# Kernel tuning notes

Hardware: AMD Instinct MI355X
Metric: run time of the kernel (lower is better)

Reference implementation:

```python
import jax, jax.numpy as jnp
import numpy as np

LEAK = 0.2
N, C, T, H, DOUT = 512, 16, 15, 32, 32


def setup_inputs() -> dict:
    key = jax.random.key(0)
    k = jax.random.split(key, 5)
    x = jax.random.normal(k[0], (N, C), dtype=jnp.float32)
    adj = jax.random.uniform(k[1], (N, N, T), dtype=jnp.float32)
    W1 = jax.random.normal(k[2], (2 * C, T + 1, H), dtype=jnp.float32) * 0.05
    W2 = jax.random.normal(k[3], (2 * C, T + 1, DOUT), dtype=jnp.float32) * 0.05
    W3 = jax.random.normal(k[4], (C, H), dtype=jnp.float32) * 0.05
    return {"x": x, "adj": adj, "W1": W1, "W2": W2, "W3": W3}


def reference(x, adj, W1, W2, W3):
    n, c = x.shape
    # input_diag: [N,N,C,1], diagonal copy of node features
    diag = jnp.einsum('mn,ni->mni', jnp.eye(n, dtype=x.dtype), x)[..., None]
    # D = concat(adj-weighted broadcast of x, diag) along edge-type axis -> [N,N,C,T+1]
    D = jnp.concatenate([jnp.einsum('mnt,ni->mnit', adj, x), diag], axis=3)
    # symmetrize along channel axis -> [N,N,2C,T+1]
    D = jnp.concatenate([D, jnp.transpose(D, (1, 0, 2, 3))], axis=2)
    K = jnp.einsum('mnit,ith->mnh', D, W1)   # [N,N,H]
    V = jnp.einsum('mnit,itd->mnd', D, W2)   # [N,N,DOUT]
    Q = x @ W3                               # [N,H]
    logits1 = jnp.einsum('nh,nmh->nm', Q, K)
    logits2 = jnp.einsum('mh,nmh->nm', Q, K)
    s1 = jax.nn.softmax(logits1, axis=1)
    s2 = jax.nn.softmax(logits2, axis=0)
    temp = jnp.einsum('nm,nmd->nd', s1, V) + jnp.einsum('nm,nmd->md', s2, V)
    return jnp.maximum(temp, LEAK * temp)  # lrelu
```

## Files before the change

kernel.cpp:

```cpp
#include <hip/hip_runtime.h>
#include <hip/hip_bf16.h>

#define NNODE 512
#define CCH   16
#define TT    15
#define TP    16
#define HH    32
#define DD    32

typedef unsigned short u16;
typedef unsigned int   u32;
typedef short bf8 __attribute__((ext_vector_type(8)));
typedef float f4  __attribute__((ext_vector_type(4)));

__device__ __forceinline__ float bf2f(u16 v) {
    union { u32 u; float f; } x; x.u = ((u32)v) << 16; return x.f;
}
__device__ __forceinline__ u16 f2bf(float f) {
    union { float f; u32 u; } x; x.f = f;
    u32 u = x.u;
    return (u16)((u + 0x7FFFu + ((u >> 16) & 1u)) >> 16);
}
__device__ __forceinline__ void unpack8(uint4 p, float* o) {
    o[0]=bf2f((u16)(p.x & 0xffffu)); o[1]=bf2f((u16)(p.x >> 16));
    o[2]=bf2f((u16)(p.y & 0xffffu)); o[3]=bf2f((u16)(p.y >> 16));
    o[4]=bf2f((u16)(p.z & 0xffffu)); o[5]=bf2f((u16)(p.z >> 16));
    o[6]=bf2f((u16)(p.w & 0xffffu)); o[7]=bf2f((u16)(p.w >> 16));
}
__device__ __forceinline__ uint4 pack8(const u16* v) {
    return make_uint4((u32)v[0]|((u32)v[1]<<16), (u32)v[2]|((u32)v[3]<<16),
                      (u32)v[4]|((u32)v[5]<<16), (u32)v[6]|((u32)v[7]<<16));
}

__global__ __launch_bounds__(256) void k_prep_adjp(
    const float* __restrict__ x, const float* __restrict__ W1,
    const float* __restrict__ W2, const float* __restrict__ W3,
    const float* __restrict__ adj,
    u16* __restrict__ A1, u16* __restrict__ B1,
    u16* __restrict__ A2, u16* __restrict__ B2,
    u16* __restrict__ A2T, u16* __restrict__ B2T,
    u16* __restrict__ Qb, float* __restrict__ QAd, float* __restrict__ QB,
    u16* __restrict__ adjP, u16* __restrict__ adjPT)
{
    int tid = threadIdx.x;
    if (blockIdx.x < 512) {
        int n = blockIdx.x;
        __shared__ alignas(16) float xs[CCH];
        __shared__ alignas(16) float A1row[512], B1row[512];
        __shared__ alignas(16) float A2row[512], B2row[512];
        __shared__ alignas(16) float Qs[HH];
        if (tid < CCH) xs[tid] = x[n*CCH + tid];
        __syncthreads();
        float xr[CCH];
        #pragma unroll
        for (int i=0;i<CCH;i++) xr[i]=xs[i];
        #pragma unroll
        for (int rep=0; rep<2; rep++) {
            int c = tid + rep*256;
            float a1=0.f,b1=0.f,a2=0.f,b2=0.f;
            #pragma unroll
            for (int i=0;i<CCH;i++) {
                a1 += xr[i]*W1[i*512 + c];
                b1 += xr[i]*W1[(CCH+i)*512 + c];
                a2 += xr[i]*W2[i*512 + c];
                b2 += xr[i]*W2[(CCH+i)*512 + c];
            }
            A1[(size_t)n*512 + c]=f2bf(a1); B1[(size_t)n*512 + c]=f2bf(b1);
            A2[(size_t)n*512 + c]=f2bf(a2); B2[(size_t)n*512 + c]=f2bf(b2);
            A1row[c]=a1; B1row[c]=b1; A2row[c]=a2; B2row[c]=b2;
        }
        if (tid < HH) {
            float q=0.f;
            #pragma unroll
            for (int i=0;i<CCH;i++) q += xr[i]*W3[i*HH + tid];
            Qs[tid]=q; Qb[(size_t)n*HH + tid]=f2bf(q);
        }
        __syncthreads();
        if (tid < TP) {
            float qa=0.f, qb=0.f;
            #pragma unroll
            for (int h=0;h<HH;h++) { qa += Qs[h]*A1row[tid*HH+h]; qb += Qs[h]*B1row[tid*HH+h]; }
            QAd[(size_t)n*TP + tid]=qa; QB[(size_t)n*TP + tid]=qb;
        }
        {
            int d = tid >> 3, t0 = (tid & 7) * 2;
            u32 pa = (u32)f2bf(A2row[t0*32 + d]) | ((u32)f2bf(A2row[(t0+1)*32 + d]) << 16);
            u32 pb = (u32)f2bf(B2row[t0*32 + d]) | ((u32)f2bf(B2row[(t0+1)*32 + d]) << 16);
            *(u32*)(A2T + (size_t)d*8192 + n*16 + t0) = pa;
            *(u32*)(B2T + (size_t)d*8192 + n*16 + t0) = pb;
        }
    } else {
        int b = blockIdx.x - 512;
        int n0 = (b >> 4) * 32, m0 = (b & 15) * 32;
        __shared__ alignas(16) u16 s[32*520];
        #pragma unroll
        for (int i = 0; i < 60; i++) {
            int e = tid + i*256;
            int nl = e / 480; int rem = e - nl*480;
            int ml = rem / 15; int t = rem - ml*15;
            float v = adj[((size_t)(n0+nl)*512 + (m0+ml))*TT + t];
            s[nl*520 + ml*16 + t] = f2bf(v);
        }
        #pragma unroll
        for (int i = 0; i < 4; i++) {
            int e = tid + i*256; int nl = e >> 5, ml = e & 31;
            s[nl*520 + ml*16 + 15] = ((n0+nl) == (m0+ml)) ? (u16)0x3F80 : (u16)0;
        }
        __syncthreads();
        #pragma unroll
        for (int i = 0; i < 8; i++) {
            int c = tid + i*256;
            int nl = c >> 6, off = (c & 63) * 8;
            uint4 vv = *(const uint4*)(s + nl*520 + off);
            *(uint4*)(adjP + (size_t)(n0+nl)*8192 + m0*16 + off) = vv;
        }
        #pragma unroll
        for (int i = 0; i < 8; i++) {
            int c = tid + i*256;
            int ml = c >> 6, nlh = c & 63, nl = nlh >> 1, half = nlh & 1;
            uint4 vv = *(const uint4*)(s + nl*520 + ml*16 + half*8);
            *(uint4*)(adjPT + (size_t)(m0+ml)*8192 + (n0+nl)*16 + half*8) = vv;
        }
    }
}

__global__ __launch_bounds__(256) void k_logits(
    const u16* __restrict__ Qb, const u16* __restrict__ A1, const u16* __restrict__ B1,
    const u16* __restrict__ adjP, const u16* __restrict__ adjPT,
    const float* __restrict__ QAd, const float* __restrict__ QB,
    float* __restrict__ L1, float* __restrict__ L2T)
{
    const int m0 = blockIdx.x * 16, n0 = blockIdx.y * 16;
    const int tid = threadIdx.x;
    const int wv = tid >> 6, lane = tid & 63, l15 = lane & 15, quad = lane >> 4;
    __shared__ alignas(16) float sL1[16*17];
    __shared__ alignas(16) float sL2[16*17];

    bf8 afragN = *(const bf8*)(Qb + (size_t)(n0 + l15)*32 + quad*8);
    bf8 afragM = *(const bf8*)(Qb + (size_t)(m0 + l15)*32 + quad*8);

    f4 accG[4], accH[4];
    #pragma unroll
    for (int j = 0; j < 4; j++) {
        int m = m0 + wv*4 + j;
        int n = n0 + wv*4 + j;
        bf8 bG = *(const bf8*)(A1 + (size_t)m*512 + l15*32 + quad*8);
        bf8 bH = *(const bf8*)(B1 + (size_t)n*512 + l15*32 + quad*8);
        f4 z = {0.f,0.f,0.f,0.f};
        accG[j] = __builtin_amdgcn_mfma_f32_16x16x32_bf16(afragN, bG, z, 0, 0, 0);
        accH[j] = __builtin_amdgcn_mfma_f32_16x16x32_bf16(afragM, bH, z, 0, 0, 0);
    }

    #pragma unroll
    for (int j = 0; j < 4; j++) {
        int m = m0 + wv*4 + j;
        #pragma unroll
        for (int r = 0; r < 4; r++) {
            int n = n0 + quad*4 + r;
            float a  = bf2f(adjP [(size_t)n*8192 + m*16 + l15]);
            float at = bf2f(adjPT[(size_t)n*8192 + m*16 + l15]);
            float v = a*accG[j][r] + at*QB[n*16 + l15];
            #pragma unroll
            for (int o = 1; o < 16; o <<= 1) v += __shfl_xor(v, o, 64);
            if (l15 == 0) sL1[(quad*4+r)*17 + wv*4 + j] = v;
        }
    }
    #pragma unroll
    for (int j = 0; j < 4; j++) {
        int n = n0 + wv*4 + j;
        #pragma unroll
        for (int r = 0; r < 4; r++) {
            int m = m0 + quad*4 + r;
            float a  = bf2f(adjP [(size_t)n*8192 + m*16 + l15]);
            float at = bf2f(adjPT[(size_t)n*8192 + m*16 + l15]);
            float v = a*QAd[m*16 + l15] + at*accH[j][r];
            #pragma unroll
            for (int o = 1; o < 16; o <<= 1) v += __shfl_xor(v, o, 64);
            if (l15 == 0) sL2[(quad*4+r)*17 + wv*4 + j] = v;
        }
    }
    __syncthreads();
    int row = tid >> 4, col = tid & 15;
    L1 [(size_t)(n0+row)*NNODE + m0 + col] = sL1[row*17+col];
    L2T[(size_t)(m0+row)*NNODE + n0 + col] = sL2[row*17+col];
}

__global__ __launch_bounds__(256) void k_softmax_w(
    const float* __restrict__ L1, const float* __restrict__ L2T,
    const u16* __restrict__ adjP, const u16* __restrict__ adjPT,
    u16* __restrict__ W1c, u16* __restrict__ W2c,
    float* __restrict__ u1, float* __restrict__ v2)
{
    int b = blockIdx.x, tid = threadIdx.x;
    bool first = b < NNODE;
    int j = first ? b : b - NNODE;
    const float* row = first ? (L1 + (size_t)j*NNODE) : (L2T + (size_t)j*NNODE);
    u16* W  = (first ? W1c : W2c) + (size_t)j*8192;
    float* uv = (first ? u1 : v2) + (size_t)j*TP;

    float v0 = row[tid], v1 = row[tid+256];
    float mx = fmaxf(v0, v1);
    #pragma unroll
    for (int o=32; o; o>>=1) mx = fmaxf(mx, __shfl_xor(mx, o, 64));
    __shared__ alignas(16) float red[4], red2[4], ur[4][16];
    int lane = tid & 63, wv = tid >> 6;
    if (!lane) red[wv] = mx;
    __syncthreads();
    mx = fmaxf(fmaxf(red[0],red[1]), fmaxf(red[2],red[3]));
    float e0 = __expf(v0 - mx), e1 = __expf(v1 - mx);
    float sm = e0 + e1;
    #pragma unroll
    for (int o=32; o; o>>=1) sm += __shfl_xor(sm, o, 64);
    if (!lane) red2[wv] = sm;
    __syncthreads();
    float inv = 1.0f / (red2[0]+red2[1]+red2[2]+red2[3]);
    float sa = e0*inv, sb = e1*inv;

    const u16* ap = adjP  + (size_t)j*8192;
    const u16* tp = adjPT + (size_t)j*8192;
    float u[16];
    #pragma unroll
    for (int t=0;t<16;t++) u[t]=0.f;
    #pragma unroll
    for (int half = 0; half < 2; half++) {
        int k = tid + half*256;
        float sv = half ? sb : sa;
        const uint4* p = (const uint4*)(ap + k*16);
        float av[16]; unpack8(p[0], av); unpack8(p[1], av+8);
        u16 o16[16];
        #pragma unroll
        for (int t=0;t<16;t++) o16[t] = f2bf(sv*av[t]);
        uint4* wp = (uint4*)(W + k*16);
        wp[0] = pack8(o16); wp[1] = pack8(o16+8);
        const uint4* q = (const uint4*)(tp + k*16);
        float tv[16]; unpack8(q[0], tv); unpack8(q[1], tv+8);
        #pragma unroll
        for (int t=0;t<16;t++) u[t] = fmaf(sv, tv[t], u[t]);
    }
    #pragma unroll
    for (int t=0;t<16;t++) {
        #pragma unroll
        for (int o=32; o; o>>=1) u[t] += __shfl_xor(u[t], o, 64);
    }
    if (!lane) {
        #pragma unroll
        for (int t=0;t<16;t++) ur[wv][t] = u[t];
    }
    __syncthreads();
    if (tid < 16) uv[tid] = ur[0][tid]+ur[1][tid]+ur[2][tid]+ur[3][tid];
}

__global__ __launch_bounds__(256) void k_gemm2(
    const u16* __restrict__ W1c, const u16* __restrict__ W2c,
    const u16* __restrict__ A2T, const u16* __restrict__ B2T,
    float* __restrict__ tempP)
{
    int tid = threadIdx.x;
    int wv = tid >> 6, lane = tid & 63, l15 = lane & 15, quad = lane >> 4;
    int w = blockIdx.x*4 + wv;
    int kc = w & 15, dt = (w >> 4) & 1, jt = w >> 5;
    size_t aRow = (size_t)(jt*16 + l15)*8192;
    size_t bRow = (size_t)(dt*16 + l15)*8192;
    int kt0 = kc*512 + quad*8;
    f4 acc = {0.f, 0.f, 0.f, 0.f};
    #pragma unroll
    for (int s = 0; s < 16; s++) {
        int kt = kt0 + s*32;
        bf8 aw1 = *(const bf8*)(W1c + aRow + kt);
        bf8 ba2 = *(const bf8*)(A2T + bRow + kt);
        acc = __builtin_amdgcn_mfma_f32_16x16x32_bf16(aw1, ba2, acc, 0, 0, 0);
        bf8 aw2 = *(const bf8*)(W2c + aRow + kt);
        bf8 bb2 = *(const bf8*)(B2T + bRow + kt);
        acc = __builtin_amdgcn_mfma_f32_16x16x32_bf16(aw2, bb2, acc, 0, 0, 0);
    }
    #pragma unroll
    for (int r = 0; r < 4; r++)
        tempP[((size_t)kc*NNODE + jt*16 + quad*4 + r)*DD + dt*16 + l15] = acc[r];
}

__global__ __launch_bounds__(256) void k_final(
    const float* __restrict__ tempP, const float* __restrict__ u1, const float* __restrict__ v2,
    const u16* __restrict__ A2, const u16* __restrict__ B2, float* __restrict__ out)
{
    int j0 = blockIdx.x * 8;
    int tid = threadIdx.x;
    int j = tid >> 5, d = tid & 31;
    int jj = j0 + j;
    float acc = 0.f;
    #pragma unroll
    for (int kc=0;kc<16;kc++) acc += tempP[((size_t)kc*NNODE + jj)*DD + d];
    #pragma unroll
    for (int t=0;t<TP;t++) {
        acc += u1[(size_t)jj*TP + t] * bf2f(B2[(size_t)jj*512 + t*32 + d]);
        acc += v2[(size_t)jj*TP + t] * bf2f(A2[(size_t)jj*512 + t*32 + d]);
    }
    out[(size_t)jj*DD + d] = fmaxf(acc, 0.2f*acc);
}

extern "C" void kernel_launch(void* const* d_in, const int* in_sizes, int n_in,
                              void* d_out, int out_size, void* d_ws, size_t ws_size,
                              hipStream_t stream)
{
    (void)in_sizes; (void)n_in; (void)out_size; (void)ws_size;
    const float* x   = (const float*)d_in[0];
    const float* adj = (const float*)d_in[1];
    const float* W1  = (const float*)d_in[2];
    const float* W2  = (const float*)d_in[3];
    const float* W3  = (const float*)d_in[4];

    char* ws = (char*)d_ws;
    u16*   adjP = (u16*)(ws);
    u16*   adjPT= (u16*)(ws + 0x800000);
    u16*   W1c  = (u16*)(ws + 0x1000000);
    u16*   W2c  = (u16*)(ws + 0x1800000);
    u16*   A1   = (u16*)(ws + 0x2000000);
    u16*   B1   = (u16*)(ws + 0x2080000);
    u16*   A2   = (u16*)(ws + 0x2100000);
    u16*   B2   = (u16*)(ws + 0x2180000);
    u16*   A2T  = (u16*)(ws + 0x2200000);
    u16*   B2T  = (u16*)(ws + 0x2280000);
    u16*   Qb   = (u16*)(ws + 0x2300000);
    float* QAd  = (float*)(ws + 0x2310000);
    float* QB   = (float*)(ws + 0x2320000);
    float* u1   = (float*)(ws + 0x2330000);
    float* v2   = (float*)(ws + 0x2340000);
    float* L1   = (float*)(ws + 0x2400000);
    float* L2T  = (float*)(ws + 0x2500000);
    float* tempP= (float*)(ws + 0x2600000);

    k_prep_adjp<<<768, 256, 0, stream>>>(x, W1, W2, W3, adj,
                                         A1, B1, A2, B2, A2T, B2T, Qb, QAd, QB, adjP, adjPT);
    k_logits<<<dim3(32,32), 256, 0, stream>>>(Qb, A1, B1, adjP, adjPT, QAd, QB, L1, L2T);
    k_softmax_w<<<1024, 256, 0, stream>>>(L1, L2T, adjP, adjPT, W1c, W2c, u1, v2);
    k_gemm2<<<256, 256, 0, stream>>>(W1c, W2c, A2T, B2T, tempP);
    k_final<<<64, 256, 0, stream>>>(tempP, u1, v2, A2, B2, (float*)d_out);
}
```

Before: 115.5 us.

## Fuse all stages into one cooperative kernel with grid-wide syncs

Merges the prep, logits, softmax-weighting, GEMM and final epilogue kernels into a single persistent cooperative kernel with 512 blocks, separated by grid.sync. The goal is to remove kernel launch gaps and the tempP partial-sum buffer, computing the self term from the A2T/B2T layout instead of separate A2/B2 arrays. In exchange, the final GEMM runs on only 16 blocks, each with a long serial K loop and no split-K. This may leave the machine underused and limit bandwidth while streaming the large W1c/W2c matrices.

```diff
diff --git a/kernel.cpp b/kernel.cpp
--- a/kernel.cpp
+++ b/kernel.cpp
@@ -1,5 +1,8 @@
 #include <hip/hip_runtime.h>
 #include <hip/hip_bf16.h>
+#include <hip/hip_cooperative_groups.h>
+
+namespace cg = cooperative_groups;
 
 #define NNODE 512
 #define CCH   16
@@ -32,23 +35,33 @@
                       (u32)v[4]|((u32)v[5]<<16), (u32)v[6]|((u32)v[7]<<16));
 }
 
-__global__ __launch_bounds__(256) void k_prep_adjp(
-    const float* __restrict__ x, const float* __restrict__ W1,
-    const float* __restrict__ W2, const float* __restrict__ W3,
-    const float* __restrict__ adj,
+__global__ __launch_bounds__(256, 2) void k_fused(
+    const float* __restrict__ x, const float* __restrict__ adj,
+    const float* __restrict__ W1, const float* __restrict__ W2,
+    const float* __restrict__ W3,
     u16* __restrict__ A1, u16* __restrict__ B1,
-    u16* __restrict__ A2, u16* __restrict__ B2,
     u16* __restrict__ A2T, u16* __restrict__ B2T,
     u16* __restrict__ Qb, float* __restrict__ QAd, float* __restrict__ QB,
-    u16* __restrict__ adjP, u16* __restrict__ adjPT)
+    u16* __restrict__ adjP, u16* __restrict__ adjPT,
+    float* __restrict__ L1, float* __restrict__ L2T,
+    u16* __restrict__ W1c, u16* __restrict__ W2c,
+    float* __restrict__ u1, float* __restrict__ v2,
+    float* __restrict__ out)
 {
-    int tid = threadIdx.x;
-    if (blockIdx.x < 512) {
-        int n = blockIdx.x;
-        __shared__ alignas(16) float xs[CCH];
-        __shared__ alignas(16) float A1row[512], B1row[512];
-        __shared__ alignas(16) float A2row[512], B2row[512];
-        __shared__ alignas(16) float Qs[HH];
+    cg::grid_group grid = cg::this_grid();
+    const int tid = threadIdx.x;
+    const int b = blockIdx.x;
+    __shared__ alignas(16) u16 sbuf[32*520];
+    float* fb = (float*)sbuf;
+
+    {
+        int n = b;
+        float* xs    = fb;
+        float* Qs    = fb + 16;
+        float* A1row = fb + 48;
+        float* B1row = fb + 560;
+        float* A2row = fb + 1072;
+        float* B2row = fb + 1584;
         if (tid < CCH) xs[tid] = x[n*CCH + tid];
         __syncthreads();
         float xr[CCH];
@@ -66,7 +79,6 @@
                 b2 += xr[i]*W2[(CCH+i)*512 + c];
             }
             A1[(size_t)n*512 + c]=f2bf(a1); B1[(size_t)n*512 + c]=f2bf(b1);
-            A2[(size_t)n*512 + c]=f2bf(a2); B2[(size_t)n*512 + c]=f2bf(b2);
             A1row[c]=a1; B1row[c]=b1; A2row[c]=a2; B2row[c]=b2;
         }
         if (tid < HH) {
@@ -89,212 +101,202 @@
             *(u32*)(A2T + (size_t)d*8192 + n*16 + t0) = pa;
             *(u32*)(B2T + (size_t)d*8192 + n*16 + t0) = pb;
         }
-    } else {
-        int b = blockIdx.x - 512;
-        int n0 = (b >> 4) * 32, m0 = (b & 15) * 32;
-        __shared__ alignas(16) u16 s[32*520];
-        #pragma unroll
-        for (int i = 0; i < 60; i++) {
-            int e = tid + i*256;
-            int nl = e / 480; int rem = e - nl*480;
-            int ml = rem / 15; int t = rem - ml*15;
-            float v = adj[((size_t)(n0+nl)*512 + (m0+ml))*TT + t];
-            s[nl*520 + ml*16 + t] = f2bf(v);
-        }
-        #pragma unroll
-        for (int i = 0; i < 4; i++) {
-            int e = tid + i*256; int nl = e >> 5, ml = e & 31;
-            s[nl*520 + ml*16 + 15] = ((n0+nl) == (m0+ml)) ? (u16)0x3F80 : (u16)0;
-        }
         __syncthreads();
-        #pragma unroll
-        for (int i = 0; i < 8; i++) {
-            int c = tid + i*256;
-            int nl = c >> 6, off = (c & 63) * 8;
-            uint4 vv = *(const uint4*)(s + nl*520 + off);
-            *(uint4*)(adjP + (size_t)(n0+nl)*8192 + m0*16 + off) = vv;
-        }
-        #pragma unroll
-        for (int i = 0; i < 8; i++) {
-            int c = tid + i*256;
-            int ml = c >> 6, nlh = c & 63, nl = nlh >> 1, half = nlh & 1;
-            uint4 vv = *(const uint4*)(s + nl*520 + ml*16 + half*8);
-            *(uint4*)(adjPT + (size_t)(m0+ml)*8192 + (n0+nl)*16 + half*8) = vv;
+        if (b < 256) {
+            int n0 = (b >> 4) * 32, m0 = (b & 15) * 32;
+            u16* s = sbuf;
+            #pragma unroll
+            for (int i = 0; i < 60; i++) {
+                int e = tid + i*256;
+                int nl = e / 480; int rem = e - nl*480;
+                int ml = rem / 15; int t = rem - ml*15;
+                float v = adj[((size_t)(n0+nl)*512 + (m0+ml))*TT + t];
+                s[nl*520 + ml*16 + t] = f2bf(v);
+            }
+            #pragma unroll
+            for (int i = 0; i < 4; i++) {
+                int e = tid + i*256; int nl = e >> 5, ml = e & 31;
+                s[nl*520 + ml*16 + 15] = ((n0+nl) == (m0+ml)) ? (u16)0x3F80 : (u16)0;
+            }
+            __syncthreads();
+            #pragma unroll
+            for (int i = 0; i < 8; i++) {
+                int c = tid + i*256;
+                int nl = c >> 6, off = (c & 63) * 8;
+                uint4 vv = *(const uint4*)(s + nl*520 + off);
+                *(uint4*)(adjP + (size_t)(n0+nl)*8192 + m0*16 + off) = vv;
+            }
+            #pragma unroll
+            for (int i = 0; i < 8; i++) {
+                int c = tid + i*256;
+                int ml = c >> 6, nlh = c & 63, nl = nlh >> 1, half = nlh & 1;
+                uint4 vv = *(const uint4*)(s + nl*520 + ml*16 + half*8);
+                *(uint4*)(adjPT + (size_t)(m0+ml)*8192 + (n0+nl)*16 + half*8) = vv;
+            }
         }
     }
-}
-
-__global__ __launch_bounds__(256) void k_logits(
-    const u16* __restrict__ Qb, const u16* __restrict__ A1, const u16* __restrict__ B1,
-    const u16* __restrict__ adjP, const u16* __restrict__ adjPT,
-    const float* __restrict__ QAd, const float* __restrict__ QB,
-    float* __restrict__ L1, float* __restrict__ L2T)
-{
-    const int m0 = blockIdx.x * 16, n0 = blockIdx.y * 16;
-    const int tid = threadIdx.x;
-    const int wv = tid >> 6, lane = tid & 63, l15 = lane & 15, quad = lane >> 4;
-    __shared__ alignas(16) float sL1[16*17];
-    __shared__ alignas(16) float sL2[16*17];
-
-    bf8 afragN = *(const bf8*)(Qb + (size_t)(n0 + l15)*32 + quad*8);
-    bf8 afragM = *(const bf8*)(Qb + (size_t)(m0 + l15)*32 + quad*8);
-
-    f4 accG[4], accH[4];
-    #pragma unroll
-    for (int j = 0; j < 4; j++) {
-        int m = m0 + wv*4 + j;
-        int n = n0 + wv*4 + j;
-        bf8 bG = *(const bf8*)(A1 + (size_t)m*512 + l15*32 + quad*8);
-        bf8 bH = *(const bf8*)(B1 + (size_t)n*512 + l15*32 + quad*8);
-        f4 z = {0.f,0.f,0.f,0.f};
-        accG[j] = __builtin_amdgcn_mfma_f32_16x16x32_bf16(afragN, bG, z, 0, 0, 0);
-        accH[j] = __builtin_amdgcn_mfma_f32_16x16x32_bf16(afragM, bH, z, 0, 0, 0);
+    grid.sync();
+
+    {
+        const int wv = tid >> 6, lane = tid & 63, l15 = lane & 15, quad = lane >> 4;
+        float* sL1 = fb;
+        float* sL2 = fb + 16*17;
+        #pragma unroll
+        for (int it = 0; it < 2; it++) {
+            __syncthreads();
+            int tile = b + it*512;
+            int m0 = (tile & 31) * 16, n0 = (tile >> 5) * 16;
+
+            bf8 afragN = *(const bf8*)(Qb + (size_t)(n0 + l15)*32 + quad*8);
+            bf8 afragM = *(const bf8*)(Qb + (size_t)(m0 + l15)*32 + quad*8);
+            f4 accG[4], accH[4];
+            #pragma unroll
+            for (int j = 0; j < 4; j++) {
+                int m = m0 + wv*4 + j;
+                int n = n0 + wv*4 + j;
+                bf8 bG = *(const bf8*)(A1 + (size_t)m*512 + l15*32 + quad*8);
+                bf8 bH = *(const bf8*)(B1 + (size_t)n*512 + l15*32 + quad*8);
+                f4 z = {0.f,0.f,0.f,0.f};
+                accG[j] = __builtin_amdgcn_mfma_f32_16x16x32_bf16(afragN, bG, z, 0, 0, 0);
+                accH[j] = __builtin_amdgcn_mfma_f32_16x16x32_bf16(afragM, bH, z, 0, 0, 0);
+            }
+            #pragma unroll
+            for (int j = 0; j < 4; j++) {
+                int m = m0 + wv*4 + j;
+                #pragma unroll
+                for (int r = 0; r < 4; r++) {
+                    int n = n0 + quad*4 + r;
+                    float a  = bf2f(adjP [(size_t)n*8192 + m*16 + l15]);
+                    float at = bf2f(adjPT[(size_t)n*8192 + m*16 + l15]);
+                    float v = a*accG[j][r] + at*QB[n*16 + l15];
+                    #pragma unroll
+                    for (int o = 1; o < 16; o <<= 1) v += __shfl_xor(v, o, 64);
+                    if (l15 == 0) sL1[(quad*4+r)*17 + wv*4 + j] = v;
+                }
+            }
+            #pragma unroll
+            for (int j = 0; j < 4; j++) {
+                int n = n0 + wv*4 + j;
+                #pragma unroll
+                for (int r = 0; r < 4; r++) {
+                    int m = m0 + quad*4 + r;
+                    float a  = bf2f(adjP [(size_t)n*8192 + m*16 + l15]);
+                    float at = bf2f(adjPT[(size_t)n*8192 + m*16 + l15]);
+                    float v = a*QAd[m*16 + l15] + at*accH[j][r];
+                    #pragma unroll
+                    for (int o = 1; o < 16; o <<= 1) v += __shfl_xor(v, o, 64);
+                    if (l15 == 0) sL2[(quad*4+r)*17 + wv*4 + j] = v;
+                }
+            }
+            __syncthreads();
+            int row = tid >> 4, col = tid & 15;
+            L1 [(size_t)(n0+row)*NNODE + m0 + col] = sL1[row*17+col];
+            L2T[(size_t)(m0+row)*NNODE + n0 + col] = sL2[row*17+col];
+        }
     }
-
-    #pragma unroll
-    for (int j = 0; j < 4; j++) {
-        int m = m0 + wv*4 + j;
+    grid.sync();
+
+    {
+        int lane = tid & 63, wv = tid >> 6;
+        float* red  = fb;
+        float* red2 = fb + 4;
+        float (*ur)[16] = (float(*)[16])(fb + 8);
+        #pragma unroll
+        for (int rr = 0; rr < 2; rr++) {
+            __syncthreads();
+            int task = b + rr*512;
+            bool first = task < NNODE;
+            int j = first ? task : task - NNODE;
+            const float* row = first ? (L1 + (size_t)j*NNODE) : (L2T + (size_t)j*NNODE);
+            u16* W  = (first ? W1c : W2c) + (size_t)j*8192;
+            float* uv = (first ? u1 : v2) + (size_t)j*TP;
+
+            float v0 = row[tid], v1 = row[tid+256];
+            float mx = fmaxf(v0, v1);
+            #pragma unroll
+            for (int o=32; o; o>>=1) mx = fmaxf(mx, __shfl_xor(mx, o, 64));
+            if (!lane) red[wv] = mx;
+            __syncthreads();
+            mx = fmaxf(fmaxf(red[0],red[1]), fmaxf(red[2],red[3]));
+            float e0 = __expf(v0 - mx), e1 = __expf(v1 - mx);
+            float sm = e0 + e1;
+            #pragma unroll
+            for (int o=32; o; o>>=1) sm += __shfl_xor(sm, o, 64);
+            if (!lane) red2[wv] = sm;
+            __syncthreads();
+            float inv = 1.0f / (red2[0]+red2[1]+red2[2]+red2[3]);
+            float sa = e0*inv, sb = e1*inv;
+
+            const u16* ap = adjP  + (size_t)j*8192;
+            const u16* tp = adjPT + (size_t)j*8192;
+            float u[16];
+            #pragma unroll
+            for (int t=0;t<16;t++) u[t]=0.f;
+            #pragma unroll
+            for (int half = 0; half < 2; half++) {
+                int k = tid + half*256;
+                float sv = half ? sb : sa;
+                const uint4* p = (const uint4*)(ap + k*16);
+                float av[16]; unpack8(p[0], av); unpack8(p[1], av+8);
+                u16 o16[16];
+                #pragma unroll
+                for (int t=0;t<16;t++) o16[t] = f2bf(sv*av[t]);
+                uint4* wp = (uint4*)(W + k*16);
+                wp[0] = pack8(o16); wp[1] = pack8(o16+8);
+                const uint4* q = (const uint4*)(tp + k*16);
+                float tv[16]; unpack8(q[0], tv); unpack8(q[1], tv+8);
+                #pragma unroll
+                for (int t=0;t<16;t++) u[t] = fmaf(sv, tv[t], u[t]);
+            }
+            #pragma unroll
+            for (int t=0;t<16;t++) {
+                #pragma unroll
+                for (int o=32; o; o>>=1) u[t] += __shfl_xor(u[t], o, 64);
+            }
+            if (!lane) {
+                #pragma unroll
+                for (int t=0;t<16;t++) ur[wv][t] = u[t];
+            }
+            __syncthreads();
+            if (tid < 16) uv[tid] = ur[0][tid]+ur[1][tid]+ur[2][tid]+ur[3][tid];
+        }
+    }
+    grid.sync();
+
+    if (b < 16) {
+        int wv = tid >> 6, lane = tid & 63, l15 = lane & 15, quad = lane >> 4;
+        int w = b*4 + wv;
+        int jt = w >> 1, dt = w & 1;
+        size_t aRow = (size_t)(jt*16 + l15)*8192;
+        size_t bRow = (size_t)(dt*16 + l15)*8192;
+        f4 acc = {0.f, 0.f, 0.f, 0.f};
+        #pragma unroll 8
+        for (int s = 0; s < 256; s++) {
+            int kt = s*32 + quad*8;
+            bf8 aw1 = *(const bf8*)(W1c + aRow + kt);
+            bf8 ba2 = *(const bf8*)(A2T + bRow + kt);
+            acc = __builtin_amdgcn_mfma_f32_16x16x32_bf16(aw1, ba2, acc, 0, 0, 0);
+            bf8 aw2 = *(const bf8*)(W2c + aRow + kt);
+            bf8 bb2 = *(const bf8*)(B2T + bRow + kt);
+            acc = __builtin_amdgcn_mfma_f32_16x16x32_bf16(aw2, bb2, acc, 0, 0, 0);
+        }
+        int d = dt*16 + l15;
         #pragma unroll
         for (int r = 0; r < 4; r++) {
-            int n = n0 + quad*4 + r;
-            float a  = bf2f(adjP [(size_t)n*8192 + m*16 + l15]);
-            float at = bf2f(adjPT[(size_t)n*8192 + m*16 + l15]);
-            float v = a*accG[j][r] + at*QB[n*16 + l15];
-            #pragma unroll
-            for (int o = 1; o < 16; o <<= 1) v += __shfl_xor(v, o, 64);
-            if (l15 == 0) sL1[(quad*4+r)*17 + wv*4 + j] = v;
+            int j = jt*16 + quad*4 + r;
+            const uint4* pb2 = (const uint4*)(B2T + (size_t)d*8192 + j*16);
+            const uint4* pa2 = (const uint4*)(A2T + (size_t)d*8192 + j*16);
+            float bv[16], av[16];
+            unpack8(pb2[0], bv); unpack8(pb2[1], bv+8);
+            unpack8(pa2[0], av); unpack8(pa2[1], av+8);
+            float self = 0.f;
+            #pragma unroll
+            for (int t = 0; t < 16; t++)
+                self += u1[(size_t)j*TP + t]*bv[t] + v2[(size_t)j*TP + t]*av[t];
+            float val = acc[r] + self;
+            out[(size_t)j*DD + d] = fmaxf(val, 0.2f*val);
         }
     }
-    #pragma unroll
-    for (int j = 0; j < 4; j++) {
-        int n = n0 + wv*4 + j;
-        #pragma unroll
-        for (int r = 0; r < 4; r++) {
-            int m = m0 + quad*4 + r;
-            float a  = bf2f(adjP [(size_t)n*8192 + m*16 + l15]);
-            float at = bf2f(adjPT[(size_t)n*8192 + m*16 + l15]);
-            float v = a*QAd[m*16 + l15] + at*accH[j][r];
-            #pragma unroll
-            for (int o = 1; o < 16; o <<= 1) v += __shfl_xor(v, o, 64);
-            if (l15 == 0) sL2[(quad*4+r)*17 + wv*4 + j] = v;
-        }
-    }
-    __syncthreads();
-    int row = tid >> 4, col = tid & 15;
-    L1 [(size_t)(n0+row)*NNODE + m0 + col] = sL1[row*17+col];
-    L2T[(size_t)(m0+row)*NNODE + n0 + col] = sL2[row*17+col];
-}
-
-__global__ __launch_bounds__(256) void k_softmax_w(
-    const float* __restrict__ L1, const float* __restrict__ L2T,
-    const u16* __restrict__ adjP, const u16* __restrict__ adjPT,
-    u16* __restrict__ W1c, u16* __restrict__ W2c,
-    float* __restrict__ u1, float* __restrict__ v2)
-{
-    int b = blockIdx.x, tid = threadIdx.x;
-    bool first = b < NNODE;
-    int j = first ? b : b - NNODE;
-    const float* row = first ? (L1 + (size_t)j*NNODE) : (L2T + (size_t)j*NNODE);
-    u16* W  = (first ? W1c : W2c) + (size_t)j*8192;
-    float* uv = (first ? u1 : v2) + (size_t)j*TP;
-
-    float v0 = row[tid], v1 = row[tid+256];
-    float mx = fmaxf(v0, v1);
-    #pragma unroll
-    for (int o=32; o; o>>=1) mx = fmaxf(mx, __shfl_xor(mx, o, 64));
-    __shared__ alignas(16) float red[4], red2[4], ur[4][16];
-    int lane = tid & 63, wv = tid >> 6;
-    if (!lane) red[wv] = mx;
-    __syncthreads();
-    mx = fmaxf(fmaxf(red[0],red[1]), fmaxf(red[2],red[3]));
-    float e0 = __expf(v0 - mx), e1 = __expf(v1 - mx);
-    float sm = e0 + e1;
-    #pragma unroll
-    for (int o=32; o; o>>=1) sm += __shfl_xor(sm, o, 64);
-    if (!lane) red2[wv] = sm;
-    __syncthreads();
-    float inv = 1.0f / (red2[0]+red2[1]+red2[2]+red2[3]);
-    float sa = e0*inv, sb = e1*inv;
-
-    const u16* ap = adjP  + (size_t)j*8192;
-    const u16* tp = adjPT + (size_t)j*8192;
-    float u[16];
-    #pragma unroll
-    for (int t=0;t<16;t++) u[t]=0.f;
-    #pragma unroll
-    for (int half = 0; half < 2; half++) {
-        int k = tid + half*256;
-        float sv = half ? sb : sa;
-        const uint4* p = (const uint4*)(ap + k*16);
-        float av[16]; unpack8(p[0], av); unpack8(p[1], av+8);
-        u16 o16[16];
-        #pragma unroll
-        for (int t=0;t<16;t++) o16[t] = f2bf(sv*av[t]);
-        uint4* wp = (uint4*)(W + k*16);
-        wp[0] = pack8(o16); wp[1] = pack8(o16+8);
-        const uint4* q = (const uint4*)(tp + k*16);
-        float tv[16]; unpack8(q[0], tv); unpack8(q[1], tv+8);
-        #pragma unroll
-        for (int t=0;t<16;t++) u[t] = fmaf(sv, tv[t], u[t]);
-    }
-    #pragma unroll
-    for (int t=0;t<16;t++) {
-        #pragma unroll
-        for (int o=32; o; o>>=1) u[t] += __shfl_xor(u[t], o, 64);
-    }
-    if (!lane) {
-        #pragma unroll
-        for (int t=0;t<16;t++) ur[wv][t] = u[t];
-    }
-    __syncthreads();
-    if (tid < 16) uv[tid] = ur[0][tid]+ur[1][tid]+ur[2][tid]+ur[3][tid];
-}
-
-__global__ __launch_bounds__(256) void k_gemm2(
-    const u16* __restrict__ W1c, const u16* __restrict__ W2c,
-    const u16* __restrict__ A2T, const u16* __restrict__ B2T,
-    float* __restrict__ tempP)
-{
-    int tid = threadIdx.x;
-    int wv = tid >> 6, lane = tid & 63, l15 = lane & 15, quad = lane >> 4;
-    int w = blockIdx.x*4 + wv;
-    int kc = w & 15, dt = (w >> 4) & 1, jt = w >> 5;
-    size_t aRow = (size_t)(jt*16 + l15)*8192;
-    size_t bRow = (size_t)(dt*16 + l15)*8192;
-    int kt0 = kc*512 + quad*8;
-    f4 acc = {0.f, 0.f, 0.f, 0.f};
-    #pragma unroll
-    for (int s = 0; s < 16; s++) {
-        int kt = kt0 + s*32;
-        bf8 aw1 = *(const bf8*)(W1c + aRow + kt);
-        bf8 ba2 = *(const bf8*)(A2T + bRow + kt);
-        acc = __builtin_amdgcn_mfma_f32_16x16x32_bf16(aw1, ba2, acc, 0, 0, 0);
-        bf8 aw2 = *(const bf8*)(W2c + aRow + kt);
-        bf8 bb2 = *(const bf8*)(B2T + bRow + kt);
-        acc = __builtin_amdgcn_mfma_f32_16x16x32_bf16(aw2, bb2, acc, 0, 0, 0);
-    }
-    #pragma unroll
-    for (int r = 0; r < 4; r++)
-        tempP[((size_t)kc*NNODE + jt*16 + quad*4 + r)*DD + dt*16 + l15] = acc[r];
-}
-
-__global__ __launch_bounds__(256) void k_final(
-    const float* __restrict__ tempP, const float* __restrict__ u1, const float* __restrict__ v2,
-    const u16* __restrict__ A2, const u16* __restrict__ B2, float* __restrict__ out)
-{
-    int j0 = blockIdx.x * 8;
-    int tid = threadIdx.x;
-    int j = tid >> 5, d = tid & 31;
-    int jj = j0 + j;
-    float acc = 0.f;
-    #pragma unroll
-    for (int kc=0;kc<16;kc++) acc += tempP[((size_t)kc*NNODE + jj)*DD + d];
-    #pragma unroll
-    for (int t=0;t<TP;t++) {
-        acc += u1[(size_t)jj*TP + t] * bf2f(B2[(size_t)jj*512 + t*32 + d]);
-        acc += v2[(size_t)jj*TP + t] * bf2f(A2[(size_t)jj*512 + t*32 + d]);
-    }
-    out[(size_t)jj*DD + d] = fmaxf(acc, 0.2f*acc);
 }
 
 extern "C" void kernel_launch(void* const* d_in, const int* in_sizes, int n_in,
@@ -315,23 +317,23 @@
     u16*   W2c  = (u16*)(ws + 0x1800000);
     u16*   A1   = (u16*)(ws + 0x2000000);
     u16*   B1   = (u16*)(ws + 0x2080000);
-    u16*   A2   = (u16*)(ws + 0x2100000);
-    u16*   B2   = (u16*)(ws + 0x2180000);
-    u16*   A2T  = (u16*)(ws + 0x2200000);
-    u16*   B2T  = (u16*)(ws + 0x2280000);
-    u16*   Qb   = (u16*)(ws + 0x2300000);
-    float* QAd  = (float*)(ws + 0x2310000);
-    float* QB   = (float*)(ws + 0x2320000);
-    float* u1   = (float*)(ws + 0x2330000);
-    float* v2   = (float*)(ws + 0x2340000);
-    float* L1   = (float*)(ws + 0x2400000);
-    float* L2T  = (float*)(ws + 0x2500000);
-    float* tempP= (float*)(ws + 0x2600000);
-
-    k_prep_adjp<<<768, 256, 0, stream>>>(x, W1, W2, W3, adj,
-                                         A1, B1, A2, B2, A2T, B2T, Qb, QAd, QB, adjP, adjPT);
-    k_logits<<<dim3(32,32), 256, 0, stream>>>(Qb, A1, B1, adjP, adjPT, QAd, QB, L1, L2T);
-    k_softmax_w<<<1024, 256, 0, stream>>>(L1, L2T, adjP, adjPT, W1c, W2c, u1, v2);
-    k_gemm2<<<256, 256, 0, stream>>>(W1c, W2c, A2T, B2T, tempP);
-    k_final<<<64, 256, 0, stream>>>(tempP, u1, v2, A2, B2, (float*)d_out);
-}
+    u16*   A2T  = (u16*)(ws + 0x2100000);
+    u16*   B2T  = (u16*)(ws + 0x2180000);
+    u16*   Qb   = (u16*)(ws + 0x2200000);
+    float* QAd  = (float*)(ws + 0x2210000);
+    float* QB   = (float*)(ws + 0x2220000);
+    float* u1   = (float*)(ws + 0x2230000);
+    float* v2   = (float*)(ws + 0x2240000);
+    float* L1   = (float*)(ws + 0x2300000);
+    float* L2T  = (float*)(ws + 0x2400000);
+    float* outp = (float*)d_out;
+
+    void* args[] = {
+        (void*)&x, (void*)&adj, (void*)&W1, (void*)&W2, (void*)&W3,
+        (void*)&A1, (void*)&B1, (void*)&A2T, (void*)&B2T,
+        (void*)&Qb, (void*)&QAd, (void*)&QB, (void*)&adjP, (void*)&adjPT,
+        (void*)&L1, (void*)&L2T, (void*)&W1c, (void*)&W2c,
+        (void*)&u1, (void*)&v2, (void*)&outp
+    };
+    hipLaunchCooperativeKernel((void*)k_fused, dim3(512), dim3(256), args, 0, stream);
+}
```

Measured after the change: 418.9 us. 3.63x slower.

## Fuse split-K GEMM reduction and final epilogue into one kernel

Applied to the files above, without the earlier changes.

Merges the split-K MFMA GEMM and the final reduction/epilogue kernel into a single 1024-thread block per output tile. The 16 K-chunk partials are now reduced in shared memory rather than written to and reread from a global tempP buffer, and the self-term reads the transposed A2T/B2T arrays so the separate A2/B2 writes in prep are dropped. This saves one kernel launch and a global round trip, but cuts the GEMM grid from 256 blocks of 256 threads to 64 blocks of 1024, which may lower occupancy spread across CUs.

```diff
diff --git a/kernel.cpp b/kernel.cpp
--- a/kernel.cpp
+++ b/kernel.cpp
@@ -37,7 +37,6 @@
     const float* __restrict__ W2, const float* __restrict__ W3,
     const float* __restrict__ adj,
     u16* __restrict__ A1, u16* __restrict__ B1,
-    u16* __restrict__ A2, u16* __restrict__ B2,
     u16* __restrict__ A2T, u16* __restrict__ B2T,
     u16* __restrict__ Qb, float* __restrict__ QAd, float* __restrict__ QB,
     u16* __restrict__ adjP, u16* __restrict__ adjPT)
@@ -66,7 +65,6 @@
                 b2 += xr[i]*W2[(CCH+i)*512 + c];
             }
             A1[(size_t)n*512 + c]=f2bf(a1); B1[(size_t)n*512 + c]=f2bf(b1);
-            A2[(size_t)n*512 + c]=f2bf(a2); B2[(size_t)n*512 + c]=f2bf(b2);
             A1row[c]=a1; B1row[c]=b1; A2row[c]=a2; B2row[c]=b2;
         }
         if (tid < HH) {
@@ -250,18 +248,20 @@
     if (tid < 16) uv[tid] = ur[0][tid]+ur[1][tid]+ur[2][tid]+ur[3][tid];
 }
 
-__global__ __launch_bounds__(256) void k_gemm2(
+__global__ __launch_bounds__(1024) void k_gemm2f(
     const u16* __restrict__ W1c, const u16* __restrict__ W2c,
     const u16* __restrict__ A2T, const u16* __restrict__ B2T,
-    float* __restrict__ tempP)
-{
-    int tid = threadIdx.x;
-    int wv = tid >> 6, lane = tid & 63, l15 = lane & 15, quad = lane >> 4;
-    int w = blockIdx.x*4 + wv;
-    int kc = w & 15, dt = (w >> 4) & 1, jt = w >> 5;
+    const float* __restrict__ u1, const float* __restrict__ v2,
+    float* __restrict__ out)
+{
+    const int tid = threadIdx.x;
+    const int wv = tid >> 6, lane = tid & 63, l15 = lane & 15, quad = lane >> 4;
+    const int jt = blockIdx.x >> 1, dt = blockIdx.x & 1;
+    __shared__ alignas(16) float sred[16][272];
+
     size_t aRow = (size_t)(jt*16 + l15)*8192;
     size_t bRow = (size_t)(dt*16 + l15)*8192;
-    int kt0 = kc*512 + quad*8;
+    int kt0 = wv*512 + quad*8;
     f4 acc = {0.f, 0.f, 0.f, 0.f};
     #pragma unroll
     for (int s = 0; s < 16; s++) {
@@ -275,26 +275,26 @@
     }
     #pragma unroll
     for (int r = 0; r < 4; r++)
-        tempP[((size_t)kc*NNODE + jt*16 + quad*4 + r)*DD + dt*16 + l15] = acc[r];
-}
-
-__global__ __launch_bounds__(256) void k_final(
-    const float* __restrict__ tempP, const float* __restrict__ u1, const float* __restrict__ v2,
-    const u16* __restrict__ A2, const u16* __restrict__ B2, float* __restrict__ out)
-{
-    int j0 = blockIdx.x * 8;
-    int tid = threadIdx.x;
-    int j = tid >> 5, d = tid & 31;
-    int jj = j0 + j;
-    float acc = 0.f;
-    #pragma unroll
-    for (int kc=0;kc<16;kc++) acc += tempP[((size_t)kc*NNODE + jj)*DD + d];
-    #pragma unroll
-    for (int t=0;t<TP;t++) {
-        acc += u1[(size_t)jj*TP + t] * bf2f(B2[(size_t)jj*512 + t*32 + d]);
-        acc += v2[(size_t)jj*TP + t] * bf2f(A2[(size_t)jj*512 + t*32 + d]);
-    }
-    out[(size_t)jj*DD + d] = fmaxf(acc, 0.2f*acc);
+        sred[wv][(quad*4+r)*17 + l15] = acc[r];
+    __syncthreads();
+    if (tid < 256) {
+        int row = tid >> 4, col = tid & 15;
+        float a = 0.f;
+        #pragma unroll
+        for (int w = 0; w < 16; w++) a += sred[w][row*17 + col];
+        int j = jt*16 + row, d = dt*16 + col;
+        const uint4* pb2 = (const uint4*)(B2T + (size_t)d*8192 + j*16);
+        const uint4* pa2 = (const uint4*)(A2T + (size_t)d*8192 + j*16);
+        float bv[16], av[16];
+        unpack8(pb2[0], bv); unpack8(pb2[1], bv+8);
+        unpack8(pa2[0], av); unpack8(pa2[1], av+8);
+        float self = 0.f;
+        #pragma unroll
+        for (int t = 0; t < 16; t++)
+            self += u1[(size_t)j*TP + t]*bv[t] + v2[(size_t)j*TP + t]*av[t];
+        float val = a + self;
+        out[(size_t)j*DD + d] = fmaxf(val, 0.2f*val);
+    }
 }
 
 extern "C" void kernel_launch(void* const* d_in, const int* in_sizes, int n_in,
@@ -315,23 +315,19 @@
     u16*   W2c  = (u16*)(ws + 0x1800000);
     u16*   A1   = (u16*)(ws + 0x2000000);
     u16*   B1   = (u16*)(ws + 0x2080000);
-    u16*   A2   = (u16*)(ws + 0x2100000);
-    u16*   B2   = (u16*)(ws + 0x2180000);
-    u16*   A2T  = (u16*)(ws + 0x2200000);
-    u16*   B2T  = (u16*)(ws + 0x2280000);
-    u16*   Qb   = (u16*)(ws + 0x2300000);
-    float* QAd  = (float*)(ws + 0x2310000);
-    float* QB   = (float*)(ws + 0x2320000);
-    float* u1   = (float*)(ws + 0x2330000);
-    float* v2   = (float*)(ws + 0x2340000);
-    float* L1   = (float*)(ws + 0x2400000);
-    float* L2T  = (float*)(ws + 0x2500000);
-    float* tempP= (float*)(ws + 0x2600000);
+    u16*   A2T  = (u16*)(ws + 0x2100000);
+    u16*   B2T  = (u16*)(ws + 0x2180000);
+    u16*   Qb   = (u16*)(ws + 0x2200000);
+    float* QAd  = (float*)(ws + 0x2210000);
+    float* QB   = (float*)(ws + 0x2220000);
+    float* u1   = (float*)(ws + 0x2230000);
+    float* v2   = (float*)(ws + 0x2240000);
+    float* L1   = (float*)(ws + 0x2300000);
+    float* L2T  = (float*)(ws + 0x2400000);
 
     k_prep_adjp<<<768, 256, 0, stream>>>(x, W1, W2, W3, adj,
-                                         A1, B1, A2, B2, A2T, B2T, Qb, QAd, QB, adjP, adjPT);
+                                         A1, B1, A2T, B2T, Qb, QAd, QB, adjP, adjPT);
     k_logits<<<dim3(32,32), 256, 0, stream>>>(Qb, A1, B1, adjP, adjPT, QAd, QB, L1, L2T);
     k_softmax_w<<<1024, 256, 0, stream>>>(L1, L2T, adjP, adjPT, W1c, W2c, u1, v2);
-    k_gemm2<<<256, 256, 0, stream>>>(W1c, W2c, A2T, B2T, tempP);
-    k_final<<<64, 256, 0, stream>>>(tempP, u1, v2, A2, B2, (float*)d_out);
-}
+    k_gemm2f<<<64, 1024, 0, stream>>>(W1c, W2c, A2T, B2T, u1, v2, (float*)d_out);
+}
```

Result: slower. 135.8 us (+17.5%).
